# Optimization experiments

Hardware: AMD Instinct MI355X
Metric: run time of the kernel (lower is better)

## Reference

```python
import jax, jax.numpy as jnp
import numpy as np

HEAD_LENGTH = 4  # hardcoded in original source; scale = 1/sqrt(4) = 0.5
SCALE = 1.0 / HEAD_LENGTH ** 0.5
MASK_FILL = -1.0e9

B, H, S, D = 2, 12, 2048, 64


def setup_inputs() -> dict:
    key = jax.random.key(0)
    kq, kk, kv, km = jax.random.split(key, 4)
    q = jax.random.normal(kq, (B, H, S, D), dtype=jnp.float32)
    k = jax.random.normal(kk, (B, H, S, D), dtype=jnp.float32)
    v = jax.random.normal(kv, (B, H, S, D), dtype=jnp.float32)
    mask = jax.random.randint(km, (B, H, S, S), 0, 2).astype(jnp.bool_)
    return {"q": q, "k": k, "v": v, "mask": mask}


def reference(q, k, v, mask):
    # scores: [B, H, S, S]
    scores = jnp.einsum("bhqd,bhkd->bhqk", q, k) * SCALE
    scores = jnp.where(mask, MASK_FILL, scores)
    attn = jax.nn.softmax(scores, axis=-1)
    # dropout is identity in eval/deterministic mode
    context = jnp.einsum("bhqk,bhkd->bhqd", attn, v)
    return (context, attn)
```

## Files before the change

### kernel.cpp

```cpp
#include <hip/hip_runtime.h>
#include <hip/hip_bf16.h>
#include <cstdint>
#include <math.h>

#define S 2048
#define D 64
#define CTX_ELEMS ((size_t)24 * S * D)
#define SDP_SCALE 0.5f
#define MASK_FILL -1.0e9f
#define LDP 72

typedef __attribute__((ext_vector_type(8))) short   bf16x8;
typedef __attribute__((ext_vector_type(4))) float   f32x4;
typedef __attribute__((ext_vector_type(4))) unsigned short us4;

__device__ __forceinline__ unsigned short f2bf(float x) {
    unsigned u = __builtin_bit_cast(unsigned, x);
    u += 0x7FFFu + ((u >> 16) & 1u);
    return (unsigned short)(u >> 16);
}
__device__ __forceinline__ float bf2f(unsigned short b) {
    unsigned u = ((unsigned)b) << 16;
    return __builtin_bit_cast(float, u);
}

__global__ __launch_bounds__(256) void sdpa_pass_a(
    const float* __restrict__ q, const float* __restrict__ k,
    const int* __restrict__ mask, float* __restrict__ out)
{
    const int t = threadIdx.x;
    const int wv = t >> 6, lane = t & 63;
    const int quad = lane >> 4, n = lane & 15;
    const int rbase = blockIdx.x * 64;
    const int bh = rbase >> 11;

    __shared__ unsigned short qhi[64 * LDP], qlo[64 * LDP];
    __shared__ unsigned short khi[64 * LDP], klo[64 * LDP];

    const float4* q4 = (const float4*)(q + (size_t)rbase * D);
    #pragma unroll
    for (int i = 0; i < 4; ++i) {
        int idx = i * 256 + t;
        int row = idx >> 4, c4 = (idx & 15) * 4;
        float4 val = q4[idx];
        float c[4] = {val.x, val.y, val.z, val.w};
        us4 h, l;
        #pragma unroll
        for (int u = 0; u < 4; ++u) {
            unsigned short hb = f2bf(c[u]);
            h[u] = hb;
            l[u] = f2bf(c[u] - bf2f(hb));
        }
        *(us4*)&qhi[row * LDP + c4] = h;
        *(us4*)&qlo[row * LDP + c4] = l;
    }
    __syncthreads();

    bf16x8 qfh[2], qfl[2];
    #pragma unroll
    for (int ks = 0; ks < 2; ++ks) {
        const unsigned short* p = &qhi[(wv * 16 + n) * LDP + ks * 32 + quad * 8];
        qfh[ks] = *(const bf16x8*)p;
        p = &qlo[(wv * 16 + n) * LDP + ks * 32 + quad * 8];
        qfl[ks] = *(const bf16x8*)p;
    }

    float m_r[4] = {-INFINITY, -INFINITY, -INFINITY, -INFINITY};
    float l_r[4] = {0.f, 0.f, 0.f, 0.f};

    const float* khead = k + (size_t)bh * S * D;
    for (int jt = 0; jt < S / 64; ++jt) {
        const float4* k4 = (const float4*)(khead + (size_t)jt * 64 * D);
        #pragma unroll
        for (int i = 0; i < 4; ++i) {
            int idx = i * 256 + t;
            int row = idx >> 4, c4 = (idx & 15) * 4;
            float4 val = k4[idx];
            float c[4] = {val.x, val.y, val.z, val.w};
            us4 h, l;
            #pragma unroll
            for (int u = 0; u < 4; ++u) {
                unsigned short hb = f2bf(c[u]);
                h[u] = hb;
                l[u] = f2bf(c[u] - bf2f(hb));
            }
            *(us4*)&khi[row * LDP + c4] = h;
            *(us4*)&klo[row * LDP + c4] = l;
        }
        __syncthreads();

        f32x4 acc[4];
        #pragma unroll
        for (int ct = 0; ct < 4; ++ct) {
            f32x4 c = {0.f, 0.f, 0.f, 0.f};
            #pragma unroll
            for (int ks = 0; ks < 2; ++ks) {
                const unsigned short* bp = &khi[(ct * 16 + n) * LDP + ks * 32 + quad * 8];
                bf16x8 bh_ = *(const bf16x8*)bp;
                bp = &klo[(ct * 16 + n) * LDP + ks * 32 + quad * 8];
                bf16x8 bl_ = *(const bf16x8*)bp;
                c = __builtin_amdgcn_mfma_f32_16x16x32_bf16(qfh[ks], bh_, c, 0, 0, 0);
                c = __builtin_amdgcn_mfma_f32_16x16x32_bf16(qfl[ks], bh_, c, 0, 0, 0);
                c = __builtin_amdgcn_mfma_f32_16x16x32_bf16(qfh[ks], bl_, c, 0, 0, 0);
            }
            acc[ct] = c;
        }

        #pragma unroll
        for (int r = 0; r < 4; ++r) {
            const int rowg = rbase + wv * 16 + quad * 4 + r;
            const int* mrowp = mask + (size_t)rowg * S + jt * 64;
            float* arowp = out + CTX_ELEMS + (size_t)rowg * S + jt * 64;
            float vals[4];
            float vmax = -INFINITY;
            #pragma unroll
            for (int ct = 0; ct < 4; ++ct) {
                float s = acc[ct][r] * SDP_SCALE;
                if (mrowp[ct * 16 + n] != 0) s = MASK_FILL;
                arowp[ct * 16 + n] = s;
                vals[ct] = s;
                vmax = fmaxf(vmax, s);
            }
            #pragma unroll
            for (int off = 1; off < 16; off <<= 1)
                vmax = fmaxf(vmax, __shfl_xor(vmax, off, 64));
            float mnew = fmaxf(m_r[r], vmax);
            float ssum = 0.f;
            #pragma unroll
            for (int ct = 0; ct < 4; ++ct) ssum += __expf(vals[ct] - mnew);
            #pragma unroll
            for (int off = 1; off < 16; off <<= 1)
                ssum += __shfl_xor(ssum, off, 64);
            l_r[r] = l_r[r] * __expf(m_r[r] - mnew) + ssum;
            m_r[r] = mnew;
        }
        __syncthreads();
    }

    if (n == 0) {
        #pragma unroll
        for (int r = 0; r < 4; ++r) {
            const int rowg = rbase + wv * 16 + quad * 4 + r;
            out[(size_t)rowg * D + 0] = m_r[r];
            out[(size_t)rowg * D + 1] = l_r[r];
        }
    }
}

__global__ __launch_bounds__(256) void sdpa_pass_b(
    const float* __restrict__ v, float* __restrict__ out)
{
    const int t = threadIdx.x;
    const int wv = t >> 6, lane = t & 63;
    const int quad = lane >> 4, n = lane & 15;
    const int rbase = blockIdx.x * 64;
    const int bh = rbase >> 11;

    __shared__ unsigned short pS[64 * LDP];
    __shared__ float mS[64], ilS[64];

    if (t < 64) {
        mS[t]  = out[(size_t)(rbase + t) * D + 0];
        ilS[t] = 1.0f / out[(size_t)(rbase + t) * D + 1];
    }
    __syncthreads();

    float* attn = out + CTX_ELEMS;
    const float* vhead = v + (size_t)bh * S * D;

    f32x4 acc[4] = {{0.f,0.f,0.f,0.f},{0.f,0.f,0.f,0.f},
                    {0.f,0.f,0.f,0.f},{0.f,0.f,0.f,0.f}};

    for (int jt = 0; jt < S / 64; ++jt) {
        #pragma unroll
        for (int i = 0; i < 4; ++i) {
            int idx = i * 256 + t;
            int row = idx >> 4, c4 = (idx & 15) * 4;
            float4* p4 = (float4*)(attn + (size_t)(rbase + row) * S + jt * 64 + c4);
            float4 sv = *p4;
            float mm = mS[row], il = ilS[row];
            sv.x = __expf(sv.x - mm) * il;
            sv.y = __expf(sv.y - mm) * il;
            sv.z = __expf(sv.z - mm) * il;
            sv.w = __expf(sv.w - mm) * il;
            *p4 = sv;
            us4 pb = { f2bf(sv.x), f2bf(sv.y), f2bf(sv.z), f2bf(sv.w) };
            *(us4*)&pS[row * LDP + c4] = pb;
        }
        __syncthreads();

        bf16x8 af[2];
        #pragma unroll
        for (int ks = 0; ks < 2; ++ks)
            af[ks] = *(const bf16x8*)&pS[(wv * 16 + n) * LDP + ks * 32 + quad * 8];

        #pragma unroll
        for (int dt = 0; dt < 4; ++dt) {
            #pragma unroll
            for (int ks = 0; ks < 2; ++ks) {
                const int kg = jt * 64 + ks * 32 + quad * 8;
                const float* vp = vhead + (size_t)kg * D + dt * 16 + n;
                bf16x8 b;
                #pragma unroll
                for (int j = 0; j < 8; ++j) b[j] = (short)f2bf(vp[(size_t)j * D]);
                acc[dt] = __builtin_amdgcn_mfma_f32_16x16x32_bf16(af[ks], b, acc[dt], 0, 0, 0);
            }
        }
        __syncthreads();
    }

    #pragma unroll
    for (int dt = 0; dt < 4; ++dt) {
        #pragma unroll
        for (int r = 0; r < 4; ++r) {
            const int rowg = rbase + wv * 16 + quad * 4 + r;
            out[(size_t)rowg * D + dt * 16 + n] = acc[dt][r];
        }
    }
}

extern "C" void kernel_launch(void* const* d_in, const int* in_sizes, int n_in,
                              void* d_out, int out_size, void* d_ws, size_t ws_size,
                              hipStream_t stream) {
    const float* q    = (const float*)d_in[0];
    const float* k    = (const float*)d_in[1];
    const float* v    = (const float*)d_in[2];
    const int*   mask = (const int*)d_in[3];
    float* out = (float*)d_out;

    sdpa_pass_a<<<24 * S / 64, 256, 0, stream>>>(q, k, mask, out);
    sdpa_pass_b<<<24 * S / 64, 256, 0, stream>>>(v, out);
}
```

Baseline: 957.3 us.

## Fuse two-pass attention into one kernel with register-resident scores

Replaces the two-kernel scheme (raw scores written to the attention buffer, then read back, exponentiated and multiplied by V) with one kernel. Each 1024-thread block owns 16 query rows, keeps all 2048 scores per row in registers across 16 waves, and reduces row max and sum through shared memory. The attention output is then written exactly once, and the partial context products are summed with LDS atomics. This removes the global write-then-read of the score matrix, but each block now reloads and reconverts K and V per 16 rows, which means more K/V traffic and heavy register pressure.

After: 1.172 ms. +22.4%, slower.

```diff
diff --git a/kernel.cpp b/kernel.cpp
--- a/kernel.cpp
+++ b/kernel.cpp
@@ -1,18 +1,17 @@
 #include <hip/hip_runtime.h>
-#include <hip/hip_bf16.h>
 #include <cstdint>
 #include <math.h>
 
 #define S 2048
 #define D 64
-#define CTX_ELEMS ((size_t)24 * S * D)
+#define NH 24
+#define CTX_ELEMS ((size_t)NH * S * D)
 #define SDP_SCALE 0.5f
 #define MASK_FILL -1.0e9f
-#define LDP 72
+#define PBW 1032
 
 typedef __attribute__((ext_vector_type(8))) short   bf16x8;
 typedef __attribute__((ext_vector_type(4))) float   f32x4;
-typedef __attribute__((ext_vector_type(4))) unsigned short us4;
 
 __device__ __forceinline__ unsigned short f2bf(float x) {
     unsigned u = __builtin_bit_cast(unsigned, x);
@@ -24,186 +23,154 @@
     return __builtin_bit_cast(float, u);
 }
 
-__global__ __launch_bounds__(256) void sdpa_pass_a(
+__global__ __launch_bounds__(1024, 4) void sdpa_fused(
     const float* __restrict__ q, const float* __restrict__ k,
-    const int* __restrict__ mask, float* __restrict__ out)
+    const float* __restrict__ v, const int* __restrict__ mask,
+    float* __restrict__ out)
 {
-    const int t = threadIdx.x;
-    const int wv = t >> 6, lane = t & 63;
+    const int t    = threadIdx.x;
+    const int w    = t >> 6;
+    const int lane = t & 63;
     const int quad = lane >> 4, n = lane & 15;
-    const int rbase = blockIdx.x * 64;
-    const int bh = rbase >> 11;
-
-    __shared__ unsigned short qhi[64 * LDP], qlo[64 * LDP];
-    __shared__ unsigned short khi[64 * LDP], klo[64 * LDP];
-
-    const float4* q4 = (const float4*)(q + (size_t)rbase * D);
-    #pragma unroll
-    for (int i = 0; i < 4; ++i) {
-        int idx = i * 256 + t;
-        int row = idx >> 4, c4 = (idx & 15) * 4;
-        float4 val = q4[idx];
-        float c[4] = {val.x, val.y, val.z, val.w};
-        us4 h, l;
-        #pragma unroll
-        for (int u = 0; u < 4; ++u) {
+    const int rbase = blockIdx.x * 16;
+    const int bh    = rbase >> 11;
+
+    __shared__ unsigned short pb[16 * PBW];
+    __shared__ float mwS[16][16];
+    __shared__ float lwS[16][16];
+    __shared__ float MS[16];
+    __shared__ float iLS[16];
+    __shared__ float ctxred[16 * D];
+
+    ctxred[t] = 0.f;
+
+    bf16x8 qfh[2], qfl[2];
+    #pragma unroll
+    for (int ks = 0; ks < 2; ++ks) {
+        const float* qp = q + (size_t)(rbase + n) * D + ks * 32 + quad * 8;
+        float4 a = *(const float4*)qp;
+        float4 b = *(const float4*)(qp + 4);
+        float c[8] = {a.x, a.y, a.z, a.w, b.x, b.y, b.z, b.w};
+        #pragma unroll
+        for (int u = 0; u < 8; ++u) {
             unsigned short hb = f2bf(c[u]);
-            h[u] = hb;
-            l[u] = f2bf(c[u] - bf2f(hb));
-        }
-        *(us4*)&qhi[row * LDP + c4] = h;
-        *(us4*)&qlo[row * LDP + c4] = l;
+            qfh[ks][u] = (short)hb;
+            qfl[ks][u] = (short)f2bf(c[u] - bf2f(hb));
+        }
+    }
+
+    const float* khead = k + (size_t)bh * S * D;
+    const float* vhead = v + (size_t)bh * S * D;
+
+    float s_reg[8][4];
+    float m4[4] = {-INFINITY, -INFINITY, -INFINITY, -INFINITY};
+    #pragma unroll
+    for (int i = 0; i < 8; ++i) {
+        const int tile = w + 16 * i;
+        f32x4 c = {0.f, 0.f, 0.f, 0.f};
+        #pragma unroll
+        for (int ks = 0; ks < 2; ++ks) {
+            const float* kp = khead + (size_t)(tile * 16 + n) * D + ks * 32 + quad * 8;
+            float4 ka = *(const float4*)kp;
+            float4 kb = *(const float4*)(kp + 4);
+            float ce[8] = {ka.x, ka.y, ka.z, ka.w, kb.x, kb.y, kb.z, kb.w};
+            bf16x8 bh_, bl_;
+            #pragma unroll
+            for (int u = 0; u < 8; ++u) {
+                unsigned short hb = f2bf(ce[u]);
+                bh_[u] = (short)hb;
+                bl_[u] = (short)f2bf(ce[u] - bf2f(hb));
+            }
+            c = __builtin_amdgcn_mfma_f32_16x16x32_bf16(qfh[ks], bh_, c, 0, 0, 0);
+            c = __builtin_amdgcn_mfma_f32_16x16x32_bf16(qfl[ks], bh_, c, 0, 0, 0);
+            c = __builtin_amdgcn_mfma_f32_16x16x32_bf16(qfh[ks], bl_, c, 0, 0, 0);
+        }
+        const int colb = tile * 16 + n;
+        #pragma unroll
+        for (int r = 0; r < 4; ++r) {
+            float sv = c[r] * SDP_SCALE;
+            const int rowg = rbase + quad * 4 + r;
+            if (mask[(size_t)rowg * S + colb] != 0) sv = MASK_FILL;
+            s_reg[i][r] = sv;
+            m4[r] = fmaxf(m4[r], sv);
+        }
+    }
+
+    #pragma unroll
+    for (int r = 0; r < 4; ++r) {
+        #pragma unroll
+        for (int off = 1; off < 16; off <<= 1)
+            m4[r] = fmaxf(m4[r], __shfl_xor(m4[r], off, 64));
+    }
+    float l4[4] = {0.f, 0.f, 0.f, 0.f};
+    #pragma unroll
+    for (int i = 0; i < 8; ++i) {
+        #pragma unroll
+        for (int r = 0; r < 4; ++r)
+            l4[r] += __expf(s_reg[i][r] - m4[r]);
+    }
+    #pragma unroll
+    for (int r = 0; r < 4; ++r) {
+        #pragma unroll
+        for (int off = 1; off < 16; off <<= 1)
+            l4[r] += __shfl_xor(l4[r], off, 64);
+    }
+    if (n == 0) {
+        #pragma unroll
+        for (int r = 0; r < 4; ++r) {
+            mwS[w][quad * 4 + r] = m4[r];
+            lwS[w][quad * 4 + r] = l4[r];
+        }
     }
     __syncthreads();
 
-    bf16x8 qfh[2], qfl[2];
-    #pragma unroll
-    for (int ks = 0; ks < 2; ++ks) {
-        const unsigned short* p = &qhi[(wv * 16 + n) * LDP + ks * 32 + quad * 8];
-        qfh[ks] = *(const bf16x8*)p;
-        p = &qlo[(wv * 16 + n) * LDP + ks * 32 + quad * 8];
-        qfl[ks] = *(const bf16x8*)p;
-    }
-
-    float m_r[4] = {-INFINITY, -INFINITY, -INFINITY, -INFINITY};
-    float l_r[4] = {0.f, 0.f, 0.f, 0.f};
-
-    const float* khead = k + (size_t)bh * S * D;
-    for (int jt = 0; jt < S / 64; ++jt) {
-        const float4* k4 = (const float4*)(khead + (size_t)jt * 64 * D);
-        #pragma unroll
-        for (int i = 0; i < 4; ++i) {
-            int idx = i * 256 + t;
-            int row = idx >> 4, c4 = (idx & 15) * 4;
-            float4 val = k4[idx];
-            float c[4] = {val.x, val.y, val.z, val.w};
-            us4 h, l;
-            #pragma unroll
-            for (int u = 0; u < 4; ++u) {
-                unsigned short hb = f2bf(c[u]);
-                h[u] = hb;
-                l[u] = f2bf(c[u] - bf2f(hb));
-            }
-            *(us4*)&khi[row * LDP + c4] = h;
-            *(us4*)&klo[row * LDP + c4] = l;
-        }
-        __syncthreads();
-
-        f32x4 acc[4];
-        #pragma unroll
-        for (int ct = 0; ct < 4; ++ct) {
-            f32x4 c = {0.f, 0.f, 0.f, 0.f};
-            #pragma unroll
-            for (int ks = 0; ks < 2; ++ks) {
-                const unsigned short* bp = &khi[(ct * 16 + n) * LDP + ks * 32 + quad * 8];
-                bf16x8 bh_ = *(const bf16x8*)bp;
-                bp = &klo[(ct * 16 + n) * LDP + ks * 32 + quad * 8];
-                bf16x8 bl_ = *(const bf16x8*)bp;
-                c = __builtin_amdgcn_mfma_f32_16x16x32_bf16(qfh[ks], bh_, c, 0, 0, 0);
-                c = __builtin_amdgcn_mfma_f32_16x16x32_bf16(qfl[ks], bh_, c, 0, 0, 0);
-                c = __builtin_amdgcn_mfma_f32_16x16x32_bf16(qfh[ks], bl_, c, 0, 0, 0);
-            }
-            acc[ct] = c;
-        }
-
-        #pragma unroll
-        for (int r = 0; r < 4; ++r) {
-            const int rowg = rbase + wv * 16 + quad * 4 + r;
-            const int* mrowp = mask + (size_t)rowg * S + jt * 64;
-            float* arowp = out + CTX_ELEMS + (size_t)rowg * S + jt * 64;
-            float vals[4];
-            float vmax = -INFINITY;
-            #pragma unroll
-            for (int ct = 0; ct < 4; ++ct) {
-                float s = acc[ct][r] * SDP_SCALE;
-                if (mrowp[ct * 16 + n] != 0) s = MASK_FILL;
-                arowp[ct * 16 + n] = s;
-                vals[ct] = s;
-                vmax = fmaxf(vmax, s);
-            }
-            #pragma unroll
-            for (int off = 1; off < 16; off <<= 1)
-                vmax = fmaxf(vmax, __shfl_xor(vmax, off, 64));
-            float mnew = fmaxf(m_r[r], vmax);
-            float ssum = 0.f;
-            #pragma unroll
-            for (int ct = 0; ct < 4; ++ct) ssum += __expf(vals[ct] - mnew);
-            #pragma unroll
-            for (int off = 1; off < 16; off <<= 1)
-                ssum += __shfl_xor(ssum, off, 64);
-            l_r[r] = l_r[r] * __expf(m_r[r] - mnew) + ssum;
-            m_r[r] = mnew;
-        }
-        __syncthreads();
-    }
-
-    if (n == 0) {
-        #pragma unroll
-        for (int r = 0; r < 4; ++r) {
-            const int rowg = rbase + wv * 16 + quad * 4 + r;
-            out[(size_t)rowg * D + 0] = m_r[r];
-            out[(size_t)rowg * D + 1] = l_r[r];
-        }
-    }
-}
-
-__global__ __launch_bounds__(256) void sdpa_pass_b(
-    const float* __restrict__ v, float* __restrict__ out)
-{
-    const int t = threadIdx.x;
-    const int wv = t >> 6, lane = t & 63;
-    const int quad = lane >> 4, n = lane & 15;
-    const int rbase = blockIdx.x * 64;
-    const int bh = rbase >> 11;
-
-    __shared__ unsigned short pS[64 * LDP];
-    __shared__ float mS[64], ilS[64];
-
-    if (t < 64) {
-        mS[t]  = out[(size_t)(rbase + t) * D + 0];
-        ilS[t] = 1.0f / out[(size_t)(rbase + t) * D + 1];
+    if (t < 16) {
+        float M = -INFINITY;
+        #pragma unroll
+        for (int ww = 0; ww < 16; ++ww) M = fmaxf(M, mwS[ww][t]);
+        float L = 0.f;
+        #pragma unroll
+        for (int ww = 0; ww < 16; ++ww) L += lwS[ww][t] * __expf(mwS[ww][t] - M);
+        MS[t]  = M;
+        iLS[t] = 1.0f / L;
     }
     __syncthreads();
 
     float* attn = out + CTX_ELEMS;
-    const float* vhead = v + (size_t)bh * S * D;
-
     f32x4 acc[4] = {{0.f,0.f,0.f,0.f},{0.f,0.f,0.f,0.f},
                     {0.f,0.f,0.f,0.f},{0.f,0.f,0.f,0.f}};
 
-    for (int jt = 0; jt < S / 64; ++jt) {
-        #pragma unroll
-        for (int i = 0; i < 4; ++i) {
-            int idx = i * 256 + t;
-            int row = idx >> 4, c4 = (idx & 15) * 4;
-            float4* p4 = (float4*)(attn + (size_t)(rbase + row) * S + jt * 64 + c4);
-            float4 sv = *p4;
-            float mm = mS[row], il = ilS[row];
-            sv.x = __expf(sv.x - mm) * il;
-            sv.y = __expf(sv.y - mm) * il;
-            sv.z = __expf(sv.z - mm) * il;
-            sv.w = __expf(sv.w - mm) * il;
-            *p4 = sv;
-            us4 pb = { f2bf(sv.x), f2bf(sv.y), f2bf(sv.z), f2bf(sv.w) };
-            *(us4*)&pS[row * LDP + c4] = pb;
+    #pragma unroll
+    for (int h = 0; h < 2; ++h) {
+        #pragma unroll
+        for (int ii = 0; ii < 4; ++ii) {
+            const int i    = h * 4 + ii;
+            const int tile = w + 16 * i;
+            const int colb = tile * 16 + n;
+            const int kloc = colb - h * 1024;
+            #pragma unroll
+            for (int r = 0; r < 4; ++r) {
+                const int row  = quad * 4 + r;
+                const int rowg = rbase + row;
+                float p = __expf(s_reg[i][r] - MS[row]) * iLS[row];
+                attn[(size_t)rowg * S + colb] = p;
+                pb[row * PBW + kloc] = f2bf(p);
+            }
         }
         __syncthreads();
 
-        bf16x8 af[2];
-        #pragma unroll
-        for (int ks = 0; ks < 2; ++ks)
-            af[ks] = *(const bf16x8*)&pS[(wv * 16 + n) * LDP + ks * 32 + quad * 8];
-
-        #pragma unroll
-        for (int dt = 0; dt < 4; ++dt) {
+        #pragma unroll
+        for (int ks = 0; ks < 2; ++ks) {
+            const int kloc0 = w * 64 + ks * 32 + quad * 8;
+            bf16x8 af = *(const bf16x8*)&pb[n * PBW + kloc0];
+            const int kg = h * 1024 + kloc0;
             #pragma unroll
-            for (int ks = 0; ks < 2; ++ks) {
-                const int kg = jt * 64 + ks * 32 + quad * 8;
+            for (int dt = 0; dt < 4; ++dt) {
                 const float* vp = vhead + (size_t)kg * D + dt * 16 + n;
-                bf16x8 b;
+                bf16x8 vb;
                 #pragma unroll
-                for (int j = 0; j < 8; ++j) b[j] = (short)f2bf(vp[(size_t)j * D]);
-                acc[dt] = __builtin_amdgcn_mfma_f32_16x16x32_bf16(af[ks], b, acc[dt], 0, 0, 0);
+                for (int j = 0; j < 8; ++j) vb[j] = (short)f2bf(vp[(size_t)j * D]);
+                acc[dt] = __builtin_amdgcn_mfma_f32_16x16x32_bf16(af, vb, acc[dt], 0, 0, 0);
             }
         }
         __syncthreads();
@@ -212,11 +179,12 @@
     #pragma unroll
     for (int dt = 0; dt < 4; ++dt) {
         #pragma unroll
-        for (int r = 0; r < 4; ++r) {
-            const int rowg = rbase + wv * 16 + quad * 4 + r;
-            out[(size_t)rowg * D + dt * 16 + n] = acc[dt][r];
-        }
-    }
+        for (int r = 0; r < 4; ++r)
+            atomicAdd(&ctxred[(quad * 4 + r) * D + dt * 16 + n], acc[dt][r]);
+    }
+    __syncthreads();
+
+    out[(size_t)(rbase + (t >> 6)) * D + (t & 63)] = ctxred[t];
 }
 
 extern "C" void kernel_launch(void* const* d_in, const int* in_sizes, int n_in,
@@ -228,6 +196,5 @@
     const int*   mask = (const int*)d_in[3];
     float* out = (float*)d_out;
 
-    sdpa_pass_a<<<24 * S / 64, 256, 0, stream>>>(q, k, mask, out);
-    sdpa_pass_b<<<24 * S / 64, 256, 0, stream>>>(v, out);
-}
+    sdpa_fused<<<NH * S / 16, 1024, 0, stream>>>(q, k, v, mask, out);
+}
```
